# Performance work log

Hardware: AMD Instinct MI355X
Metric: run time of the kernel (lower is better)

Reference implementation:

```python
import jax, jax.numpy as jnp
import numpy as np

N = 1024      # number of stocks
D_FEAT = 6    # features per day
T = 60        # lookback window
HID = 64      # GRU hidden size
R = 60        # number of relation types


def setup_inputs() -> dict:
    key = jax.random.key(0)
    ks = jax.random.split(key, 10)
    s = 1.0 / np.sqrt(HID)
    u = lambda k, shape: jax.random.uniform(k, shape, jnp.float32, -s, s)
    inp = {
        "x": jax.random.normal(ks[0], (N, D_FEAT * T), jnp.float32),
        "relation_matrix": (jax.random.uniform(ks[1], (N, N, R)) < 0.02).astype(jnp.float32),
        # GRU params (PyTorch layout: W_ih [3H, D], W_hh [3H, H])
        "W_ih": u(ks[2], (3 * HID, D_FEAT)),
        "W_hh": u(ks[3], (3 * HID, HID)),
        "b_ih": u(ks[4], (3 * HID,)),
        "b_hh": u(ks[5], (3 * HID,)),
        # attention linear W: Linear(2H+R, 1) -> weight vector + bias
        "w_att": jax.random.normal(ks[6], (2 * HID + R,), jnp.float32) * 0.05,
        "b_att": u(ks[7], (1,)),
        "W_fc": u(ks[8], (1, 2 * HID)),
        "b_fc": u(ks[9], (1,)),
    }
    return inp


def reference(x, relation_matrix, W_ih, W_hh, b_ih, b_hh, w_att, b_att, W_fc, b_fc):
    n = x.shape[0]
    H = W_hh.shape[1]
    # [N, D*T] -> [N, D, T] -> [N, T, D] -> [T, N, D] for scan over time
    xh = x.reshape(n, D_FEAT, -1).transpose(0, 2, 1)
    xs = jnp.transpose(xh, (1, 0, 2))

    def gru_step(h, xt):
        gi = xt @ W_ih.T + b_ih          # [N, 3H]
        gh = h @ W_hh.T + b_hh           # [N, 3H]
        i_r, i_z, i_n = jnp.split(gi, 3, axis=1)
        h_r, h_z, h_n = jnp.split(gh, 3, axis=1)
        r = jax.nn.sigmoid(i_r + h_r)
        z = jax.nn.sigmoid(i_z + h_z)
        nn_ = jnp.tanh(i_n + r * h_n)
        return (1.0 - z) * nn_ + z * h, None

    h0 = jnp.zeros((n, H), x.dtype)
    h_last, _ = jax.lax.scan(gru_step, h0, xs)  # [N, H] (last timestep)

    # concat-attention score: W([e_i || e_j || rel_ij]) decomposed to avoid
    # materializing the [N, N, 2H+R] concat tensor (same math as torch)
    w_ei, w_ej, w_rel = w_att[:H], w_att[H:2 * H], w_att[2 * H:]
    s_i = h_last @ w_ei                                   # [N]
    s_j = h_last @ w_ej                                   # [N]
    s_rel = jnp.einsum('ijr,r->ij', relation_matrix, w_rel)  # [N, N]
    weight = s_i[:, None] + s_j[None, :] + s_rel + b_att[0]
    weight = jnp.where(weight >= 0, weight, 0.01 * weight)   # LeakyReLU(0.01)

    mask = (jnp.sum(relation_matrix, axis=2) != 0).astype(x.dtype)  # [N, N]
    temp = mask * weight
    temp = jnp.where(temp == 0, jnp.asarray(-10000.0, x.dtype), temp)
    valid = jax.nn.softmax(temp, axis=1) * mask

    agg = valid @ h_last                                  # [N, H]
    hidden = jnp.concatenate([h_last, agg], axis=1)       # [N, 2H]
    out = (hidden @ W_fc.T + b_fc)[:, 0]                  # [N]
    return out
```

## Files before the change

kernel.cpp:

```cpp
#include <hip/hip_runtime.h>

#define NN 1024
#define DFEAT 6
#define TSTEPS 60
#define HID 64
#define RREL 60
#define SENT -1.0e30f

typedef unsigned int uint4v __attribute__((ext_vector_type(4)));

__global__ __launch_bounds__(256) void fused_kernel(
    const float* __restrict__ x,
    const float* __restrict__ W_ih,
    const float* __restrict__ W_hh,
    const float* __restrict__ b_ih,
    const float* __restrict__ b_hh,
    const float* __restrict__ w_att,
    const float* __restrict__ rel,
    float* __restrict__ h_last,
    float* __restrict__ s_i,
    float* __restrict__ s_j,
    float* __restrict__ temp)
{
    if (blockIdx.x >= NN) {
        const int b = blockIdx.x - NN;
        const int i = b >> 2;
        const int j = ((b & 3) << 8) + threadIdx.x;
        const size_t pair = (size_t)i * NN + j;

        float wrel[RREL];
#pragma unroll
        for (int r = 0; r < RREL; ++r) wrel[r] = w_att[2 * HID + r];

        const uint4v* rp = reinterpret_cast<const uint4v*>(rel + pair * RREL);
        float srel = 0.0f;
        unsigned int mb = 0u;
#pragma unroll
        for (int k = 0; k < RREL / 4; ++k) {
            uint4v v = rp[k];
            srel += __uint_as_float(v.x) * wrel[4*k+0]
                  + __uint_as_float(v.y) * wrel[4*k+1]
                  + __uint_as_float(v.z) * wrel[4*k+2]
                  + __uint_as_float(v.w) * wrel[4*k+3];
            mb |= v.x | v.y | v.z | v.w;
        }
        temp[pair] = (mb != 0u) ? srel : SENT;
        return;
    }

    const int n = blockIdx.x;
    const int g = threadIdx.x;

    __shared__ __align__(16) float x_sh[DFEAT * TSTEPS];
    __shared__ __align__(16) float h_sh[HID];
    __shared__ float gi_sh[192];
    __shared__ float gh_sh[192];

    for (int idx = g; idx < DFEAT * TSTEPS; idx += 256)
        x_sh[idx] = x[(size_t)n * (DFEAT * TSTEPS) + idx];

    float whh[HID];
    float wih[DFEAT];
    float bih = 0.0f, bhh = 0.0f;
    if (g < 192) {
#pragma unroll
        for (int k4 = 0; k4 < HID / 4; ++k4) {
            float4 w = *reinterpret_cast<const float4*>(&W_hh[g * HID + k4 * 4]);
            whh[k4 * 4 + 0] = w.x; whh[k4 * 4 + 1] = w.y;
            whh[k4 * 4 + 2] = w.z; whh[k4 * 4 + 3] = w.w;
        }
#pragma unroll
        for (int d = 0; d < DFEAT; ++d) wih[d] = W_ih[g * DFEAT + d];
        bih = b_ih[g];
        bhh = b_hh[g];
    }

    if (g < HID) h_sh[g] = 0.0f;
    __syncthreads();

    for (int t = 0; t < TSTEPS; ++t) {
        if (g < 192) {
            float gi = bih;
#pragma unroll
            for (int d = 0; d < DFEAT; ++d) gi += x_sh[d * TSTEPS + t] * wih[d];

            float gh = bhh;
#pragma unroll
            for (int k4 = 0; k4 < HID / 4; ++k4) {
                float4 hv = *reinterpret_cast<const float4*>(&h_sh[k4 * 4]);
                gh += hv.x * whh[k4 * 4 + 0] + hv.y * whh[k4 * 4 + 1]
                    + hv.z * whh[k4 * 4 + 2] + hv.w * whh[k4 * 4 + 3];
            }
            gi_sh[g] = gi;
            gh_sh[g] = gh;
        }
        __syncthreads();

        if (g < HID) {
            float ir = gi_sh[g],        hr = gh_sh[g];
            float iz = gi_sh[HID + g],  hz = gh_sh[HID + g];
            float in_ = gi_sh[2*HID + g], hn = gh_sh[2*HID + g];
            float r = 1.0f / (1.0f + __expf(-(ir + hr)));
            float z = 1.0f / (1.0f + __expf(-(iz + hz)));
            float nn_ = tanhf(in_ + r * hn);
            float hold = h_sh[g];
            h_sh[g] = (1.0f - z) * nn_ + z * hold;
        }
        __syncthreads();
    }

    if (g < HID) {
        float hv = h_sh[g];
        h_last[(size_t)n * HID + g] = hv;
        float pi = hv * w_att[g];
        float pj = hv * w_att[HID + g];
#pragma unroll
        for (int off = 32; off > 0; off >>= 1) {
            pi += __shfl_down(pi, off);
            pj += __shfl_down(pj, off);
        }
        if (g == 0) { s_i[n] = pi; s_j[n] = pj; }
    }
}

__global__ __launch_bounds__(256) void row_kernel(
    const float* __restrict__ temp,
    const float* __restrict__ s_i,
    const float* __restrict__ s_j,
    const float* __restrict__ b_att,
    const float* __restrict__ h_last,
    const float* __restrict__ W_fc,
    const float* __restrict__ b_fc,
    float* __restrict__ out)
{
    const int i = blockIdx.x;
    const int tid = threadIdx.x;

    __shared__ __align__(16) float pm_sh[NN];
    __shared__ float red_sh[256];

    const float si_b = s_i[i] + b_att[0];
    float4 sv = reinterpret_cast<const float4*>(temp + (size_t)i * NN)[tid];
    float4 sj = reinterpret_cast<const float4*>(s_j)[tid];

    float tvv[4];
    {
        float srels[4] = {sv.x, sv.y, sv.z, sv.w};
        float sjs[4]   = {sj.x, sj.y, sj.z, sj.w};
#pragma unroll
        for (int c = 0; c < 4; ++c) {
            float w = si_b + sjs[c] + srels[c];
            w = (w >= 0.0f) ? w : 0.01f * w;
            float tv = (srels[c] != SENT) ? w : 0.0f;
            tvv[c] = (tv == 0.0f) ? -10000.0f : tv;
        }
    }
    float m = fmaxf(fmaxf(tvv[0], tvv[1]), fmaxf(tvv[2], tvv[3]));
    red_sh[tid] = m;
    __syncthreads();
    for (int s = 128; s > 0; s >>= 1) {
        if (tid < s) red_sh[tid] = fmaxf(red_sh[tid], red_sh[tid + s]);
        __syncthreads();
    }
    const float M = red_sh[0];
    __syncthreads();

    float lsum = 0.0f;
    float4 pmv;
    {
        float e0 = __expf(tvv[0] - M), e1 = __expf(tvv[1] - M);
        float e2 = __expf(tvv[2] - M), e3 = __expf(tvv[3] - M);
        lsum = e0 + e1 + e2 + e3;
        pmv.x = (tvv[0] != -10000.0f) ? e0 : 0.0f;
        pmv.y = (tvv[1] != -10000.0f) ? e1 : 0.0f;
        pmv.z = (tvv[2] != -10000.0f) ? e2 : 0.0f;
        pmv.w = (tvv[3] != -10000.0f) ? e3 : 0.0f;
    }
    reinterpret_cast<float4*>(pm_sh)[tid] = pmv;

    red_sh[tid] = lsum;
    __syncthreads();
    for (int s = 128; s > 0; s >>= 1) {
        if (tid < s) red_sh[tid] += red_sh[tid + s];
        __syncthreads();
    }
    const float invS = 1.0f / red_sh[0];
    __syncthreads();

    const int h = tid & (HID - 1);
    const int grp = tid >> 6;
    float part = 0.0f;
    const float* hl = h_last + (size_t)grp * 256 * HID + h;
    const float* pm = pm_sh + grp * 256;
    for (int jc = 0; jc < 256; ++jc)
        part += pm[jc] * hl[(size_t)jc * HID];

    red_sh[tid] = part;
    __syncthreads();

    if (tid < HID) {
        float agg = (red_sh[tid] + red_sh[HID + tid]
                   + red_sh[2 * HID + tid] + red_sh[3 * HID + tid]) * invS;
        float o = h_last[(size_t)i * HID + tid] * W_fc[tid] + agg * W_fc[HID + tid];
#pragma unroll
        for (int off = 32; off > 0; off >>= 1) o += __shfl_down(o, off);
        if (tid == 0) out[i] = o + b_fc[0];
    }
}

extern "C" void kernel_launch(void* const* d_in, const int* in_sizes, int n_in,
                              void* d_out, int out_size, void* d_ws, size_t ws_size,
                              hipStream_t stream) {
    const float* x     = (const float*)d_in[0];
    const float* rel   = (const float*)d_in[1];
    const float* W_ih  = (const float*)d_in[2];
    const float* W_hh  = (const float*)d_in[3];
    const float* b_ih  = (const float*)d_in[4];
    const float* b_hh  = (const float*)d_in[5];
    const float* w_att = (const float*)d_in[6];
    const float* b_att = (const float*)d_in[7];
    const float* W_fc  = (const float*)d_in[8];
    const float* b_fc  = (const float*)d_in[9];

    float* ws     = (float*)d_ws;
    float* h_last = ws;
    float* s_i    = ws + NN * HID;
    float* s_j    = ws + NN * HID + NN;
    float* temp   = ws + NN * HID + 2 * NN;

    fused_kernel<<<NN + NN * 4, 256, 0, stream>>>(
        x, W_ih, W_hh, b_ih, b_hh, w_att, rel, h_last, s_i, s_j, temp);
    row_kernel<<<NN, 256, 0, stream>>>(temp, s_i, s_j, b_att, h_last,
                                       W_fc, b_fc, (float*)d_out);
}
```

Measured before the change: 96.48 us.

## Fold fc head into per-node scalar to skip attention aggregation matvec

Precompute each node's hidden state dotted with both halves of the fc weight in the GRU kernel. The row kernel then reduces softmax numerators against the scalar h_j·W_fc2 instead of aggregating the full 64-wide hidden vectors. This removes the per-row 1024×64 gather over h_last and its cache traffic. Summation order changes, so the floating-point result may differ slightly.

```diff
diff --git a/kernel.cpp b/kernel.cpp
--- a/kernel.cpp
+++ b/kernel.cpp
@@ -16,10 +16,13 @@
     const float* __restrict__ b_ih,
     const float* __restrict__ b_hh,
     const float* __restrict__ w_att,
+    const float* __restrict__ W_fc,
     const float* __restrict__ rel,
     float* __restrict__ h_last,
     float* __restrict__ s_i,
     float* __restrict__ s_j,
+    float* __restrict__ s_f1,
+    float* __restrict__ s_hw,
     float* __restrict__ temp)
 {
     if (blockIdx.x >= NN) {
@@ -114,12 +117,16 @@
         h_last[(size_t)n * HID + g] = hv;
         float pi = hv * w_att[g];
         float pj = hv * w_att[HID + g];
+        float f1 = hv * W_fc[g];
+        float hw = hv * W_fc[HID + g];
 #pragma unroll
         for (int off = 32; off > 0; off >>= 1) {
             pi += __shfl_down(pi, off);
             pj += __shfl_down(pj, off);
-        }
-        if (g == 0) { s_i[n] = pi; s_j[n] = pj; }
+            f1 += __shfl_down(f1, off);
+            hw += __shfl_down(hw, off);
+        }
+        if (g == 0) { s_i[n] = pi; s_j[n] = pj; s_f1[n] = f1; s_hw[n] = hw; }
     }
 }
 
@@ -127,17 +134,17 @@
     const float* __restrict__ temp,
     const float* __restrict__ s_i,
     const float* __restrict__ s_j,
+    const float* __restrict__ s_f1,
+    const float* __restrict__ s_hw,
     const float* __restrict__ b_att,
-    const float* __restrict__ h_last,
-    const float* __restrict__ W_fc,
     const float* __restrict__ b_fc,
     float* __restrict__ out)
 {
     const int i = blockIdx.x;
     const int tid = threadIdx.x;
 
-    __shared__ __align__(16) float pm_sh[NN];
     __shared__ float red_sh[256];
+    __shared__ float red2_sh[256];
 
     const float si_b = s_i[i] + b_att[0];
     float4 sv = reinterpret_cast<const float4*>(temp + (size_t)i * NN)[tid];
@@ -165,47 +172,30 @@
     const float M = red_sh[0];
     __syncthreads();
 
-    float lsum = 0.0f;
-    float4 pmv;
+    float4 hw4 = reinterpret_cast<const float4*>(s_hw)[tid];
+    float lsum, pdot;
     {
         float e0 = __expf(tvv[0] - M), e1 = __expf(tvv[1] - M);
         float e2 = __expf(tvv[2] - M), e3 = __expf(tvv[3] - M);
         lsum = e0 + e1 + e2 + e3;
-        pmv.x = (tvv[0] != -10000.0f) ? e0 : 0.0f;
-        pmv.y = (tvv[1] != -10000.0f) ? e1 : 0.0f;
-        pmv.z = (tvv[2] != -10000.0f) ? e2 : 0.0f;
-        pmv.w = (tvv[3] != -10000.0f) ? e3 : 0.0f;
-    }
-    reinterpret_cast<float4*>(pm_sh)[tid] = pmv;
-
-    red_sh[tid] = lsum;
+        float p0 = (tvv[0] != -10000.0f) ? e0 : 0.0f;
+        float p1 = (tvv[1] != -10000.0f) ? e1 : 0.0f;
+        float p2 = (tvv[2] != -10000.0f) ? e2 : 0.0f;
+        float p3 = (tvv[3] != -10000.0f) ? e3 : 0.0f;
+        pdot = p0 * hw4.x + p1 * hw4.y + p2 * hw4.z + p3 * hw4.w;
+    }
+    red_sh[tid]  = lsum;
+    red2_sh[tid] = pdot;
     __syncthreads();
     for (int s = 128; s > 0; s >>= 1) {
-        if (tid < s) red_sh[tid] += red_sh[tid + s];
-        __syncthreads();
-    }
-    const float invS = 1.0f / red_sh[0];
-    __syncthreads();
-
-    const int h = tid & (HID - 1);
-    const int grp = tid >> 6;
-    float part = 0.0f;
-    const float* hl = h_last + (size_t)grp * 256 * HID + h;
-    const float* pm = pm_sh + grp * 256;
-    for (int jc = 0; jc < 256; ++jc)
-        part += pm[jc] * hl[(size_t)jc * HID];
-
-    red_sh[tid] = part;
-    __syncthreads();
-
-    if (tid < HID) {
-        float agg = (red_sh[tid] + red_sh[HID + tid]
-                   + red_sh[2 * HID + tid] + red_sh[3 * HID + tid]) * invS;
-        float o = h_last[(size_t)i * HID + tid] * W_fc[tid] + agg * W_fc[HID + tid];
-#pragma unroll
-        for (int off = 32; off > 0; off >>= 1) o += __shfl_down(o, off);
-        if (tid == 0) out[i] = o + b_fc[0];
-    }
+        if (tid < s) {
+            red_sh[tid]  += red_sh[tid + s];
+            red2_sh[tid] += red2_sh[tid + s];
+        }
+        __syncthreads();
+    }
+    if (tid == 0)
+        out[i] = s_f1[i] + b_fc[0] + red2_sh[0] / red_sh[0];
 }
 
 extern "C" void kernel_launch(void* const* d_in, const int* in_sizes, int n_in,
@@ -226,10 +216,13 @@
     float* h_last = ws;
     float* s_i    = ws + NN * HID;
     float* s_j    = ws + NN * HID + NN;
-    float* temp   = ws + NN * HID + 2 * NN;
+    float* s_f1   = ws + NN * HID + 2 * NN;
+    float* s_hw   = ws + NN * HID + 3 * NN;
+    float* temp   = ws + NN * HID + 4 * NN;
 
     fused_kernel<<<NN + NN * 4, 256, 0, stream>>>(
-        x, W_ih, W_hh, b_ih, b_hh, w_att, rel, h_last, s_i, s_j, temp);
-    row_kernel<<<NN, 256, 0, stream>>>(temp, s_i, s_j, b_att, h_last,
-                                       W_fc, b_fc, (float*)d_out);
+        x, W_ih, W_hh, b_ih, b_hh, w_att, W_fc, rel,
+        h_last, s_i, s_j, s_f1, s_hw, temp);
+    row_kernel<<<NN, 256, 0, stream>>>(temp, s_i, s_j, s_f1, s_hw,
+                                       b_att, b_fc, (float*)d_out);
 }
```

Measured after the change: 88.00 us, median of 2. -8.8%, faster.
